# Kernel tuning notes

Hardware: AMD Instinct MI355X
Metric: run time of the kernel (lower is better)

## Reference

```python
import jax, jax.numpy as jnp
import numpy as np

DIM = 512
HEADS = 8
SCALE = DIM ** (-0.5)  # scale_with_head=False


def setup_inputs() -> dict:
    key = jax.random.key(0)
    k1, k2, k3 = jax.random.split(key, 3)
    x = jax.random.normal(k1, (16, 1024, DIM), dtype=jnp.float32)
    w_qkv = jax.random.normal(k2, (DIM, 3 * DIM), dtype=jnp.float32) * (DIM ** -0.5)
    w_out = jax.random.normal(k3, (DIM, DIM), dtype=jnp.float32) * (DIM ** -0.5)
    b_out = jnp.zeros((DIM,), dtype=jnp.float32)
    return {"x": x, "w_qkv": w_qkv, "w_out": w_out, "b_out": b_out}


def reference(x, w_qkv, w_out, b_out):
    b, n, _ = x.shape
    h = HEADS
    qkv = x @ w_qkv  # [b, n, 3*dim]
    q, k, v = jnp.split(qkv, 3, axis=-1)
    # b n (h d) -> b h n d
    reshape = lambda t: t.reshape(b, n, h, -1).transpose(0, 2, 1, 3)
    q, k, v = reshape(q), reshape(k), reshape(v)
    dots = jnp.einsum('bhid,bhjd->bhij', q, k) * SCALE  # [b,h,n,n]
    attn = jax.nn.softmax(dots, axis=-1)
    out = jnp.einsum('bhij,bhjd->bhid', attn, v)
    out = out.transpose(0, 2, 1, 3).reshape(b, n, h * (DIM // h))  # b n (h d)
    return out @ w_out + b_out
```

## Files before the change

kernel.cpp:

```cpp
#include <hip/hip_runtime.h>
#include <math.h>


#define QSCALE_ 0.06376541773f
#define RESCALE_THR_ 8.0f

typedef float f32x4 __attribute__((ext_vector_type(4)));
typedef __bf16 bf16x8 __attribute__((ext_vector_type(8)));

static __device__ __forceinline__ ushort bf_bits(float f) {
    unsigned u = __builtin_bit_cast(unsigned, f);
    u += 0x7fffu + ((u >> 16) & 1u);
    return (ushort)(u >> 16);
}
static __device__ __forceinline__ unsigned cvt_pk_bf16(float lo, float hi) {
    unsigned d;
    asm("v_cvt_pk_bf16_f32 %0, %1, %2" : "=v"(d) : "v"(lo), "v"(hi));
    return d;
}

#define GLDS16(gsrc, ldst)                                                              \
    __builtin_amdgcn_global_load_lds((const __attribute__((address_space(1))) void*)(gsrc), \
                                     (__attribute__((address_space(3))) void*)(ldst), 16, 0, 0)

__global__ __launch_bounds__(256) void cast_bf16(const float* __restrict__ in,
                                                 ushort* __restrict__ out, int n4) {
    const int i = blockIdx.x * 256 + threadIdx.x;
    if (i >= n4) return;
    const float4 v = ((const float4*)in)[i];
    ushort4 o;
    o.x = bf_bits(v.x); o.y = bf_bits(v.y); o.z = bf_bits(v.z); o.w = bf_bits(v.w);
    ((ushort4*)out)[i] = o;
}

__global__ __launch_bounds__(256) void transpose_cast(const float* __restrict__ in,
                                                      ushort* __restrict__ out,
                                                      int K, int N, float scale, int scaleRows) {
    __shared__ float t[32][33];
    const int n0 = blockIdx.x * 32, k0 = blockIdx.y * 32;
    const int tx = threadIdx.x & 31, ty = threadIdx.x >> 5;
    for (int i = ty; i < 32; i += 8)
        t[i][tx] = in[(size_t)(k0 + i) * N + n0 + tx];
    __syncthreads();
    for (int i = ty; i < 32; i += 8) {
        const float s = (n0 + i < scaleRows) ? scale : 1.f;
        out[(size_t)(n0 + i) * K + k0 + tx] = bf_bits(t[tx][i] * s);
    }
}

__global__ __launch_bounds__(256) void gemm_bf16(const ushort* __restrict__ A,
                                                 const ushort* __restrict__ BT,
                                                 const float* __restrict__ bias,
                                                 float* __restrict__ C,
                                                 ushort* __restrict__ Cb,
                                                 ushort* __restrict__ VT,
                                                 int M, int N, int K) {
    __shared__ __align__(16) char lds[16384];
    const int tid = threadIdx.x;
    const int lane = tid & 63;
    const int w = tid >> 6;
    const int wr = w >> 1, wc = w & 1;
    const int fr = lane & 15;
    const int fg = lane >> 4;
    const int rowBase = blockIdx.y * 128;
    const int colBase = blockIdx.x * 128;

    f32x4 acc[4][4] = {};

    for (int k0 = 0; k0 < K; k0 += 32) {
#pragma unroll
        for (int r = 0; r < 2; ++r) {
            const unsigned boff = r * 4096u + w * 1024u + lane * 16u;
            const unsigned row = boff >> 6;
            const unsigned ke = (boff & 63u) >> 1;
            GLDS16(A + (size_t)(rowBase + row) * K + k0 + ke, lds + r * 4096 + w * 1024);
            GLDS16(BT + (size_t)(colBase + row) * K + k0 + ke, lds + 8192 + r * 4096 + w * 1024);
        }
        __syncthreads();

        bf16x8 a_frag[4], b_frag[4];
#pragma unroll
        for (int mi = 0; mi < 4; ++mi)
            a_frag[mi] = *(const bf16x8*)(lds + ((wr * 64 + mi * 16 + fr) * 64 + fg * 16));
#pragma unroll
        for (int ni = 0; ni < 4; ++ni)
            b_frag[ni] = *(const bf16x8*)(lds + 8192 + ((wc * 64 + ni * 16 + fr) * 64 + fg * 16));
#pragma unroll
        for (int mi = 0; mi < 4; ++mi)
#pragma unroll
            for (int ni = 0; ni < 4; ++ni)
                acc[mi][ni] = __builtin_amdgcn_mfma_f32_16x16x32_bf16(a_frag[mi], b_frag[ni],
                                                                      acc[mi][ni], 0, 0, 0);
        __syncthreads();
    }

#pragma unroll
    for (int ni = 0; ni < 4; ++ni) {
        const int col = colBase + wc * 64 + ni * 16 + fr;
        const float bv = bias ? bias[col] : 0.f;
#pragma unroll
        for (int mi = 0; mi < 4; ++mi) {
            const int row0 = rowBase + wr * 64 + mi * 16 + fg * 4;
            if (Cb) {
                if (VT && col >= 1024) {
                    const int hd = col - 1024;
                    const size_t vb = ((size_t)((row0 >> 10) * 8 + (hd >> 6)) * 64 + (hd & 63)) * 1024
                                      + (row0 & 1023);
                    ushort4 pk4;
                    pk4.x = bf_bits(acc[mi][ni][0]);
                    pk4.y = bf_bits(acc[mi][ni][1]);
                    pk4.z = bf_bits(acc[mi][ni][2]);
                    pk4.w = bf_bits(acc[mi][ni][3]);
                    *(ushort4*)(VT + vb) = pk4;
                } else {
#pragma unroll
                    for (int q = 0; q < 4; ++q)
                        Cb[(size_t)(row0 + q) * N + col] = bf_bits(acc[mi][ni][q]);
                }
            } else {
#pragma unroll
                for (int q = 0; q < 4; ++q)
                    C[(size_t)(row0 + q) * N + col] = acc[mi][ni][q] + bv;
            }
        }
    }
}

__global__ __launch_bounds__(256) void attn_mfma(const ushort* __restrict__ qkv,
                                                 const ushort* __restrict__ vT,
                                                 ushort* __restrict__ aoutb) {
    __shared__ __align__(16) char lds[40960];
    const int qt = blockIdx.x;
    const int bh = blockIdx.y;
    const int b = bh >> 3, h = bh & 7;
    const int tid = threadIdx.x;
    const int lane = tid & 63;
    const int w = tid >> 6;
    const int fr = lane & 15;
    const int fg = lane >> 4;

    const size_t nbase = (size_t)b * 1024;
    const int qrow0 = qt * 64;

    bf16x8 qf[2];
    {
        const size_t qa = (nbase + qrow0 + w * 16 + fr) * 1536 + h * 64;
        qf[0] = *(const bf16x8*)(qkv + qa + fg * 8);
        qf[1] = *(const bf16x8*)(qkv + qa + 32 + fg * 8);
    }

    const int srow = w * 16 + (lane >> 3);
    const int slot = lane & 7;
    auto stage = [&](int kt, int buf) {
        char* kd = lds + buf * 8192;
        char* vd = lds + 16384 + buf * 8192;
#pragma unroll
        for (int r = 0; r < 2; ++r) {
            const int row = srow + r * 8;
            const int sw = slot ^ (row & 7);
            GLDS16(qkv + (nbase + kt * 64 + row) * 1536 + 512 + h * 64 + sw * 8,
                   kd + (w * 2 + r) * 1024);
            GLDS16(vT + ((size_t)bh * 64 + row) * 1024 + kt * 64 + sw * 8,
                   vd + (w * 2 + r) * 1024);
        }
    };

    f32x4 o[4] = {};
    float mrow = -INFINITY, lrow = 0.f;

    stage(0, 0);
    __syncthreads();
    int cur = 0;
    char* const pbase = lds + 32768 + w * 2048;

    for (int kt = 0; kt < 16; ++kt) {
        if (kt < 15) stage(kt + 1, cur ^ 1);
        const char* kb = lds + cur * 8192;
        const char* vb = lds + 16384 + cur * 8192;

        f32x4 S[4];
#pragma unroll
        for (int jb = 0; jb < 4; ++jb) {
            f32x4 a = {};
#pragma unroll
            for (int s = 0; s < 2; ++s) {
                const int row = jb * 16 + fr;
                const int c = s * 64 + fg * 16;
                const bf16x8 kf = *(const bf16x8*)(kb + row * 128 + (c ^ ((row & 7) << 4)));
                a = __builtin_amdgcn_mfma_f32_16x16x32_bf16(kf, qf[s], a, 0, 0, 0);
            }
            S[jb] = a;
        }

        float tmax = -INFINITY;
#pragma unroll
        for (int jb = 0; jb < 4; ++jb)
#pragma unroll
            for (int r = 0; r < 4; ++r) tmax = fmaxf(tmax, S[jb][r]);
        tmax = fmaxf(tmax, __shfl_xor(tmax, 16));
        tmax = fmaxf(tmax, __shfl_xor(tmax, 32));

        if (!__all(tmax - mrow <= RESCALE_THR_)) {
            const float mnew = fmaxf(mrow, tmax);
            const float corr = __builtin_amdgcn_exp2f(mrow - mnew);
            mrow = mnew;
            lrow *= corr;
#pragma unroll
            for (int r = 0; r < 4; ++r) {
                const float cr = __shfl(corr, fg * 4 + r);
#pragma unroll
                for (int dvb = 0; dvb < 4; ++dvb) o[dvb][r] *= cr;
            }
        }

        float psum = 0.f;
#pragma unroll
        for (int jb = 0; jb < 4; ++jb)
#pragma unroll
            for (int r = 0; r < 4; ++r) {
                const float p = __builtin_amdgcn_exp2f(S[jb][r] - mrow);
                S[jb][r] = p;
                psum += p;
            }
        psum += __shfl_xor(psum, 16);
        psum += __shfl_xor(psum, 32);
        lrow += psum;

#pragma unroll
        for (int jb = 0; jb < 4; ++jb) {
            unsigned pk2[2];
            pk2[0] = cvt_pk_bf16(S[jb][0], S[jb][1]);
            pk2[1] = cvt_pk_bf16(S[jb][2], S[jb][3]);
            *(ulong1*)(pbase + fr * 128 + ((jb * 32 + fg * 8) ^ ((fr & 7) << 4))) =
                *(ulong1*)pk2;
        }

#pragma unroll
        for (int s = 0; s < 2; ++s) {
            const int pc = s * 64 + fg * 16;
            const bf16x8 pf = *(const bf16x8*)(pbase + fr * 128 + (pc ^ ((fr & 7) << 4)));
#pragma unroll
            for (int dvb = 0; dvb < 4; ++dvb) {
                const int vrow = dvb * 16 + fr;
                const bf16x8 vf = *(const bf16x8*)(vb + vrow * 128 + (pc ^ ((vrow & 7) << 4)));
                o[dvb] = __builtin_amdgcn_mfma_f32_16x16x32_bf16(pf, vf, o[dvb], 0, 0, 0);
            }
        }
        __syncthreads();
        cur ^= 1;
    }

#pragma unroll
    for (int r = 0; r < 4; ++r) {
        const float linv = 1.f / __shfl(lrow, fg * 4 + r);
        const size_t n = nbase + qrow0 + w * 16 + fg * 4 + r;
#pragma unroll
        for (int dvb = 0; dvb < 4; ++dvb)
            aoutb[n * 512 + h * 64 + dvb * 16 + fr] = bf_bits(o[dvb][r] * linv);
    }
}

extern "C" void kernel_launch(void* const* d_in, const int* in_sizes, int n_in,
                              void* d_out, int out_size, void* d_ws, size_t ws_size,
                              hipStream_t stream) {
    const float* x     = (const float*)d_in[0];
    const float* w_qkv = (const float*)d_in[1];
    const float* w_out = (const float*)d_in[2];
    const float* b_out = (const float*)d_in[3];
    float* out = (float*)d_out;

    char* ws = (char*)d_ws;
    ushort* qkvb  = (ushort*)ws;
    ushort* vT    = (ushort*)(ws + 50331648);
    ushort* xb    = (ushort*)(ws + 50331648 + 16777216);
    ushort* aoutb = xb;
    ushort* wqkvT = (ushort*)(ws + 50331648 + 33554432);
    ushort* woutT = (ushort*)(ws + 50331648 + 33554432 + 1572864);

    const dim3 blk(256);
    cast_bf16<<<dim3(8388608 / 4 / 256), blk, 0, stream>>>(x, xb, 8388608 / 4);
    transpose_cast<<<dim3(1536 / 32, 512 / 32), blk, 0, stream>>>(w_qkv, wqkvT, 512, 1536,
                                                                  QSCALE_, 512);
    transpose_cast<<<dim3(512 / 32, 512 / 32), blk, 0, stream>>>(w_out, woutT, 512, 512,
                                                                 1.f, 0);
    gemm_bf16<<<dim3(12, 128), blk, 0, stream>>>(xb, wqkvT, nullptr, nullptr, qkvb, vT,
                                                 16384, 1536, 512);
    attn_mfma<<<dim3(16, 128), blk, 0, stream>>>(qkvb, vT, aoutb);
    gemm_bf16<<<dim3(4, 128), blk, 0, stream>>>(aoutb, woutT, b_out, out, nullptr, nullptr,
                                                16384, 512, 512);
}
```

Baseline: 152.0 us.

## Compute softmax row sums via MFMA with ones vector and unroll KV loop by two

Replaces the scalar exp-sum and cross-lane shuffle reduction with an extra MFMA of the bf16 P tile against a vector of ones. The row sum then builds up in an accumulator laid out like the output, so the final normalization needs no shuffle. The change also fuses exp2 into the bf16 pack, uses three-input max chains, and adds s_setprio around the MFMA sections. It unrolls the KV loop by two so buffer indices are compile-time constants. The row sum now comes from bf16-rounded probabilities, which slightly changes numerics, and each tile issues two extra MFMAs.

```diff
diff --git a/kernel.cpp b/kernel.cpp
--- a/kernel.cpp
+++ b/kernel.cpp
@@ -17,6 +17,9 @@
     unsigned d;
     asm("v_cvt_pk_bf16_f32 %0, %1, %2" : "=v"(d) : "v"(lo), "v"(hi));
     return d;
+}
+static __device__ __forceinline__ float fmax3_(float a, float b, float c) {
+    return fmaxf(fmaxf(a, b), c);
 }
 
 #define GLDS16(gsrc, ldst)                                                              \
@@ -149,6 +152,10 @@
         qf[1] = *(const bf16x8*)(qkv + qa + 32 + fg * 8);
     }
 
+    bf16x8 onesf;
+#pragma unroll
+    for (int e = 0; e < 8; ++e) onesf[e] = __builtin_bit_cast(__bf16, (ushort)0x3F80);
+
     const int srow = w * 16 + (lane >> 3);
     const int slot = lane & 7;
     auto stage = [&](int kt, int buf) {
@@ -166,19 +173,20 @@
     };
 
     f32x4 o[4] = {};
-    float mrow = -INFINITY, lrow = 0.f;
+    f32x4 lacc = {};
+    float mrow = -INFINITY;
 
     stage(0, 0);
     __syncthreads();
-    int cur = 0;
     char* const pbase = lds + 32768 + w * 2048;
 
-    for (int kt = 0; kt < 16; ++kt) {
+    auto tile = [&](int kt, int cur) {
         if (kt < 15) stage(kt + 1, cur ^ 1);
         const char* kb = lds + cur * 8192;
         const char* vb = lds + 16384 + cur * 8192;
 
         f32x4 S[4];
+        __builtin_amdgcn_s_setprio(1);
 #pragma unroll
         for (int jb = 0; jb < 4; ++jb) {
             f32x4 a = {};
@@ -191,12 +199,16 @@
             }
             S[jb] = a;
         }
-
-        float tmax = -INFINITY;
-#pragma unroll
-        for (int jb = 0; jb < 4; ++jb)
-#pragma unroll
-            for (int r = 0; r < 4; ++r) tmax = fmaxf(tmax, S[jb][r]);
+        __builtin_amdgcn_s_setprio(0);
+
+        float tmax = fmax3_(S[0][0], S[0][1], S[0][2]);
+        tmax = fmax3_(tmax, S[0][3], S[1][0]);
+        tmax = fmax3_(tmax, S[1][1], S[1][2]);
+        tmax = fmax3_(tmax, S[1][3], S[2][0]);
+        tmax = fmax3_(tmax, S[2][1], S[2][2]);
+        tmax = fmax3_(tmax, S[2][3], S[3][0]);
+        tmax = fmax3_(tmax, S[3][1], S[3][2]);
+        tmax = fmaxf(tmax, S[3][3]);
         tmax = fmaxf(tmax, __shfl_xor(tmax, 16));
         tmax = fmaxf(tmax, __shfl_xor(tmax, 32));
 
@@ -204,41 +216,35 @@
             const float mnew = fmaxf(mrow, tmax);
             const float corr = __builtin_amdgcn_exp2f(mrow - mnew);
             mrow = mnew;
-            lrow *= corr;
 #pragma unroll
             for (int r = 0; r < 4; ++r) {
                 const float cr = __shfl(corr, fg * 4 + r);
+                lacc[r] *= cr;
 #pragma unroll
                 for (int dvb = 0; dvb < 4; ++dvb) o[dvb][r] *= cr;
             }
         }
 
-        float psum = 0.f;
-#pragma unroll
-        for (int jb = 0; jb < 4; ++jb)
-#pragma unroll
-            for (int r = 0; r < 4; ++r) {
-                const float p = __builtin_amdgcn_exp2f(S[jb][r] - mrow);
-                S[jb][r] = p;
-                psum += p;
-            }
-        psum += __shfl_xor(psum, 16);
-        psum += __shfl_xor(psum, 32);
-        lrow += psum;
-
 #pragma unroll
         for (int jb = 0; jb < 4; ++jb) {
-            unsigned pk2[2];
-            pk2[0] = cvt_pk_bf16(S[jb][0], S[jb][1]);
-            pk2[1] = cvt_pk_bf16(S[jb][2], S[jb][3]);
-            *(ulong1*)(pbase + fr * 128 + ((jb * 32 + fg * 8) ^ ((fr & 7) << 4))) =
-                *(ulong1*)pk2;
-        }
-
+            const unsigned lo = cvt_pk_bf16(__builtin_amdgcn_exp2f(S[jb][0] - mrow),
+                                            __builtin_amdgcn_exp2f(S[jb][1] - mrow));
+            const unsigned hi = cvt_pk_bf16(__builtin_amdgcn_exp2f(S[jb][2] - mrow),
+                                            __builtin_amdgcn_exp2f(S[jb][3] - mrow));
+            const unsigned long long pv =
+                (unsigned long long)lo | ((unsigned long long)hi << 32);
+            *(unsigned long long*)(pbase + fr * 128 +
+                                   ((jb * 32 + fg * 8) ^ ((fr & 7) << 4))) = pv;
+        }
+
+        asm volatile("" ::: "memory");
+
+        __builtin_amdgcn_s_setprio(1);
 #pragma unroll
         for (int s = 0; s < 2; ++s) {
             const int pc = s * 64 + fg * 16;
             const bf16x8 pf = *(const bf16x8*)(pbase + fr * 128 + (pc ^ ((fr & 7) << 4)));
+            lacc = __builtin_amdgcn_mfma_f32_16x16x32_bf16(pf, onesf, lacc, 0, 0, 0);
 #pragma unroll
             for (int dvb = 0; dvb < 4; ++dvb) {
                 const int vrow = dvb * 16 + fr;
@@ -246,13 +252,18 @@
                 o[dvb] = __builtin_amdgcn_mfma_f32_16x16x32_bf16(pf, vf, o[dvb], 0, 0, 0);
             }
         }
+        __builtin_amdgcn_s_setprio(0);
         __syncthreads();
-        cur ^= 1;
+    };
+
+    for (int kt = 0; kt < 16; kt += 2) {
+        tile(kt, 0);
+        tile(kt + 1, 1);
     }
 
 #pragma unroll
     for (int r = 0; r < 4; ++r) {
-        const float linv = 1.f / __shfl(lrow, fg * 4 + r);
+        const float linv = 1.f / lacc[r];
         const size_t n = nbase + qrow0 + w * 16 + fg * 4 + r;
 #pragma unroll
         for (int dvb = 0; dvb < 4; ++dvb)
```

Measured after the change: 150.1 us. About the same (-1.2%).
